# Kernel optimization log

Hardware: AMD Instinct MI355X
Metric: run time of the kernel (lower is better)

Reference implementation:

```python
import jax, jax.numpy as jnp
import numpy as np

D = 1024          # model_dim
BD = D // 2       # bottleneck_dim
K = 64            # num_splats
B, S = 8, 2048


def setup_inputs() -> dict:
    key = jax.random.key(0)
    ks = jax.random.split(key, 12)
    sc = 0.02
    return {
        "token_embeddings": jax.random.normal(ks[0], (B, S, D), jnp.float32),
        "splat_influences": jax.random.uniform(ks[1], (B, S, K), jnp.float32),
        # encoder: Linear(D -> BD), stored [in, out]
        "enc_W": jax.random.normal(ks[2], (D, BD), jnp.float32) * sc,
        "enc_b": jnp.zeros((BD,), jnp.float32),
        # per-splat transforms: K x Linear(BD -> BD)
        "trans_W": jax.random.normal(ks[3], (K, BD, BD), jnp.float32) * sc,
        "trans_b": jnp.zeros((K, BD), jnp.float32),
        # decoder: Linear(BD -> D)
        "dec_W": jax.random.normal(ks[4], (BD, D), jnp.float32) * sc,
        "dec_b": jnp.zeros((D,), jnp.float32),
        # flow gate: Linear(D -> D) + sigmoid
        "gate_W": jax.random.normal(ks[5], (D, D), jnp.float32) * sc,
        "gate_b": jnp.zeros((D,), jnp.float32),
    }


def reference(token_embeddings, splat_influences, enc_W, enc_b,
              trans_W, trans_b, dec_W, dec_b, gate_W, gate_b):
    # gather: [B,K,S] @ [B,S,D] -> [B,K,D]
    influences_t = jnp.swapaxes(splat_influences, 1, 2)          # [B,K,S]
    gathered = jnp.einsum('bks,bsd->bkd', influences_t, token_embeddings)
    total = jnp.clip(influences_t.sum(axis=2, keepdims=True), 1e-8, None)  # [B,K,1]
    gathered = gathered / total
    # encoder (dropout inactive at eval)
    encoded = jax.nn.relu(gathered @ enc_W + enc_b)              # [B,K,BD]
    # per-splat transform as grouped matmul
    transformed = jnp.einsum('bkd,kde->bke', encoded, trans_W) + trans_b  # [B,K,BD]
    decoded = transformed @ dec_W + dec_b                        # [B,K,D]
    # scatter back to tokens: [B,S,K] @ [B,K,D]
    flow = jnp.einsum('bsk,bkd->bsd', splat_influences, decoded)
    gate = jax.nn.sigmoid(token_embeddings @ gate_W + gate_b)    # [B,S,D]
    return flow * gate
```

## Files before the change

kernel.cpp:

```cpp
#include <hip/hip_runtime.h>

#define BB 8
#define SS 2048
#define DD 1024
#define BDD 512
#define NSP 64

typedef __attribute__((ext_vector_type(8))) short bf16x8;
typedef __attribute__((ext_vector_type(4))) float f32x4;
typedef unsigned short u16;
typedef unsigned int u32;

__device__ __forceinline__ u16 f2bf(float f) {
  u32 u = __builtin_bit_cast(u32, f);
  u = u + 0x7fffu + ((u >> 16) & 1u);
  return (u16)(u >> 16);
}

__device__ __forceinline__ void gl_lds16(const void* g, void* l) {
  __builtin_amdgcn_global_load_lds((const __attribute__((address_space(1))) void*)g,
                                   (__attribute__((address_space(3))) void*)l,
                                   16, 0, 0);
}

__global__ void k_prep(const float* __restrict__ tok, const float* __restrict__ infl,
                       const float* __restrict__ gw, u16* __restrict__ tokbf,
                       u16* __restrict__ tokT, u16* __restrict__ inflbf,
                       u16* __restrict__ inflT, float* __restrict__ rsum,
                       u16* __restrict__ gwt) {
  __shared__ __align__(16) char smraw[128 * 41 * 4];
  u16(*tile)[80] = (u16(*)[80])smraw;
  float(*ps)[64] = (float(*)[64])(smraw + 64 * 80 * 2);
  float(*gt)[33] = (float(*)[33])smraw;
  int bid = blockIdx.x;
  int t = threadIdx.x;

  if (bid < 2048) {
    u32* t32 = (u32*)smraw;
    int C0 = (bid & 15) * 64;
    int R0 = (bid >> 4) * 128;
    int b = R0 >> 11, s0 = R0 & 2047;
    int lc = (t & 7) * 8;
#pragma unroll
    for (int i = 0; i < 4; ++i) {
      int r = (t >> 3) + i * 32;
      const float* src = tok + (size_t)(R0 + r) * DD + C0 + lc;
      float4 a = *(const float4*)src;
      float4 bq = *(const float4*)(src + 4);
      uint4 v;
      v.x = f2bf(a.x) | ((u32)f2bf(a.y) << 16);
      v.y = f2bf(a.z) | ((u32)f2bf(a.w) << 16);
      v.z = f2bf(bq.x) | ((u32)f2bf(bq.y) << 16);
      v.w = f2bf(bq.z) | ((u32)f2bf(bq.w) << 16);
      *(uint4*)(tokbf + (size_t)(R0 + r) * DD + C0 + lc) = v;
      int cbase = r * 41 + (t & 7) * 4;
      t32[cbase + 0] = v.x;
      t32[cbase + 1] = v.y;
      t32[cbase + 2] = v.z;
      t32[cbase + 3] = v.w;
    }
    __syncthreads();
    int dp = t >> 3;
    size_t tb = (size_t)b * DD * SS;
#pragma unroll
    for (int h = 0; h < 2; ++h) {
      int sseg = (t & 7) * 8 + h * 64;
      u32 w[8];
#pragma unroll
      for (int j = 0; j < 8; ++j) w[j] = t32[(sseg + j) * 41 + dp];
      uint4 vlo, vhi;
      vlo.x = (w[0] & 0xffffu) | (w[1] << 16);
      vlo.y = (w[2] & 0xffffu) | (w[3] << 16);
      vlo.z = (w[4] & 0xffffu) | (w[5] << 16);
      vlo.w = (w[6] & 0xffffu) | (w[7] << 16);
      vhi.x = (w[0] >> 16) | (w[1] & 0xffff0000u);
      vhi.y = (w[2] >> 16) | (w[3] & 0xffff0000u);
      vhi.z = (w[4] >> 16) | (w[5] & 0xffff0000u);
      vhi.w = (w[6] >> 16) | (w[7] & 0xffff0000u);
      *(uint4*)(tokT + tb + (size_t)(C0 + 2 * dp) * SS + s0 + sseg) = vlo;
      *(uint4*)(tokT + tb + (size_t)(C0 + 2 * dp + 1) * SS + s0 + sseg) = vhi;
    }
  } else if (bid < 2304) {
    int R0 = (bid - 2048) * 64;
    int b = R0 >> 11, s0 = R0 & 2047;
    int st = s0 >> 6;
    int lr = t >> 3, lc = (t & 7) * 8;
    float col[8];
#pragma unroll
    for (int j = 0; j < 8; ++j) col[j] = 0.f;
#pragma unroll
    for (int i = 0; i < 2; ++i) {
      int r = lr + i * 32;
      const float* src = infl + (size_t)(R0 + r) * NSP + lc;
      float4 a = *(const float4*)src;
      float4 bq = *(const float4*)(src + 4);
      col[0] += a.x; col[1] += a.y; col[2] += a.z; col[3] += a.w;
      col[4] += bq.x; col[5] += bq.y; col[6] += bq.z; col[7] += bq.w;
      uint4 v;
      v.x = f2bf(a.x) | ((u32)f2bf(a.y) << 16);
      v.y = f2bf(a.z) | ((u32)f2bf(a.w) << 16);
      v.z = f2bf(bq.x) | ((u32)f2bf(bq.y) << 16);
      v.w = f2bf(bq.z) | ((u32)f2bf(bq.w) << 16);
      *(uint4*)(inflbf + (size_t)(R0 + r) * NSP + lc) = v;
      *(uint4*)&tile[r][lc] = v;
    }
#pragma unroll
    for (int j = 0; j < 8; ++j) ps[lr][lc + j] = col[j];
    __syncthreads();
    if (t < 64) {
      float s = 0.f;
#pragma unroll
      for (int rr = 0; rr < 32; ++rr) s += ps[rr][t];
      rsum[((size_t)b * 32 + st) * 64 + t] = s;
    }
    int sseg = (t & 7) * 8;
#pragma unroll
    for (int i = 0; i < 2; ++i) {
      int dcol = (t >> 3) + i * 32;
      u16 a0 = tile[sseg + 0][dcol], a1 = tile[sseg + 1][dcol];
      u16 a2 = tile[sseg + 2][dcol], a3 = tile[sseg + 3][dcol];
      u16 a4 = tile[sseg + 4][dcol], a5 = tile[sseg + 5][dcol];
      u16 a6 = tile[sseg + 6][dcol], a7 = tile[sseg + 7][dcol];
      uint4 v;
      v.x = a0 | ((u32)a1 << 16);
      v.y = a2 | ((u32)a3 << 16);
      v.z = a4 | ((u32)a5 << 16);
      v.w = a6 | ((u32)a7 << 16);
      *(uint4*)(inflT + ((size_t)b * NSP + dcol) * SS + s0 + sseg) = v;
    }
  } else {
    int g = bid - 2304;
    int n0 = (g & 31) * 32, k0 = (g >> 5) * 32;
    int tx = t & 31, ty = t >> 5;
#pragma unroll
    for (int r = 0; r < 4; ++r) {
      int kr = ty + r * 8;
      gt[kr][tx] = gw[(k0 + kr) * DD + n0 + tx];
    }
    __syncthreads();
#pragma unroll
    for (int r = 0; r < 4; ++r) {
      int nc = ty + r * 8;
      gwt[(n0 + nc) * DD + k0 + tx] = f2bf(gt[tx][nc]);
    }
  }
}

__global__ __launch_bounds__(256) void k_gather_mfma(const u16* __restrict__ inflT,
                                                     const u16* __restrict__ tokT,
                                                     float* __restrict__ pg) {
  __shared__ u16 As[64 * 64];
  __shared__ u16 Bs[64 * 64];
  int t = threadIdx.x;
  int l = t & 63, w = t >> 6;
  int wr = w >> 1, wc = w & 1;
  int n0 = blockIdx.x * 64;
  int b = blockIdx.y;
  int sq = blockIdx.z;
  int l15 = l & 15, lh = l >> 4;
  int srow = t >> 3, scol = (t & 7) * 8;

  const u16* ap = inflT + (size_t)b * NSP * SS;
  const u16* bp = tokT + (size_t)b * DD * SS;

  f32x4 acc[2][2];
#pragma unroll
  for (int i = 0; i < 2; ++i)
#pragma unroll
    for (int j = 0; j < 2; ++j) acc[i][j] = (f32x4){0.f, 0.f, 0.f, 0.f};

  for (int kt = 0; kt < 8; ++kt) {
    int k0 = sq * 512 + kt * 64;
#pragma unroll
    for (int i = 0; i < 2; ++i) {
      int row = srow + i * 32;
      gl_lds16(ap + row * SS + k0 + scol, &As[row * 64 + scol]);
      gl_lds16(bp + (n0 + row) * SS + k0 + scol, &Bs[row * 64 + scol]);
    }
    __syncthreads();
#pragma unroll
    for (int ks = 0; ks < 2; ++ks) {
      bf16x8 af[2], bfv[2];
#pragma unroll
      for (int mi = 0; mi < 2; ++mi)
        af[mi] = *(const bf16x8*)&As[(wr * 32 + mi * 16 + l15) * 64 + ks * 32 + lh * 8];
#pragma unroll
      for (int ni = 0; ni < 2; ++ni)
        bfv[ni] = *(const bf16x8*)&Bs[(wc * 32 + ni * 16 + l15) * 64 + ks * 32 + lh * 8];
#pragma unroll
      for (int mi = 0; mi < 2; ++mi)
#pragma unroll
        for (int ni = 0; ni < 2; ++ni)
          acc[mi][ni] = __builtin_amdgcn_mfma_f32_16x16x32_bf16(af[mi], bfv[ni], acc[mi][ni], 0, 0, 0);
    }
    __syncthreads();
  }

#pragma unroll
  for (int mi = 0; mi < 2; ++mi)
#pragma unroll
    for (int ni = 0; ni < 2; ++ni)
#pragma unroll
      for (int r = 0; r < 4; ++r) {
        int krow = wr * 32 + mi * 16 + lh * 4 + r;
        int dcol = n0 + wc * 32 + ni * 16 + l15;
        pg[((size_t)sq * 512 + b * NSP + krow) * DD + dcol] = acc[mi][ni][r];
      }
}

__global__ void k_enc_part(const float* __restrict__ pg, const float* __restrict__ rsum,
                           const float* __restrict__ encW, float* __restrict__ pe) {
  __shared__ float gl[8][64];
  int dq = blockIdx.x, mt = blockIdx.y;
  int m0 = mt * 8, d0 = dq * 64;
  int t = threadIdx.x;
  {
    int r = t >> 5, c = t & 31;
    float s1 = 0.f, s2 = 0.f;
#pragma unroll
    for (int q = 0; q < 4; ++q) {
      const float* qp = pg + ((size_t)q * 512 + m0 + r) * DD + d0;
      s1 += qp[c]; s2 += qp[c + 32];
    }
    int mrow = m0 + r;
    int bq = mrow >> 6, kq = mrow & 63;
    float tt = 0.f;
#pragma unroll
    for (int st = 0; st < 32; ++st) tt += rsum[((size_t)bq * 32 + st) * 64 + kq];
    float rt = 1.f / fmaxf(tt, 1e-8f);
    gl[r][c] = s1 * rt;
    gl[r][c + 32] = s2 * rt;
  }
  __syncthreads();
  int n4 = (t & 127) * 4, mh = (t >> 7) * 4;
  float4 acc[4];
#pragma unroll
  for (int m = 0; m < 4; ++m) acc[m] = (float4){0.f, 0.f, 0.f, 0.f};
  for (int i = 0; i < 64; ++i) {
    float4 wv = *(const float4*)(encW + (d0 + i) * BDD + n4);
#pragma unroll
    for (int m = 0; m < 4; ++m) {
      float g = gl[mh + m][i];
      acc[m].x += g * wv.x; acc[m].y += g * wv.y;
      acc[m].z += g * wv.z; acc[m].w += g * wv.w;
    }
  }
#pragma unroll
  for (int m = 0; m < 4; ++m)
    *(float4*)(pe + ((size_t)dq * 512 + m0 + mh + m) * BDD + n4) = acc[m];
}

__global__ void k_trans_part(const float* __restrict__ pe, const float* __restrict__ encB,
                             const float* __restrict__ trW, float* __restrict__ pt) {
  __shared__ float el[8][32];
  int dq = blockIdx.x, ks = blockIdx.y;
  int d0 = dq * 32;
  int t = threadIdx.x;
  {
    int r = t >> 5, c = t & 31;
    int m = r * NSP + ks;
    float s = 0.f;
#pragma unroll
    for (int p = 0; p < 16; ++p)
      s += pe[((size_t)p * 512 + m) * BDD + d0 + c];
    el[r][c] = fmaxf(s + encB[d0 + c], 0.f);
  }
  __syncthreads();
  int n4 = (t & 127) * 4, mh = (t >> 7) * 4;
  float4 acc[4];
#pragma unroll
  for (int m = 0; m < 4; ++m) acc[m] = (float4){0.f, 0.f, 0.f, 0.f};
  for (int i = 0; i < 32; ++i) {
    float4 wv = *(const float4*)(trW + ((size_t)ks * BDD + d0 + i) * BDD + n4);
#pragma unroll
    for (int m = 0; m < 4; ++m) {
      float g = el[mh + m][i];
      acc[m].x += g * wv.x; acc[m].y += g * wv.y;
      acc[m].z += g * wv.z; acc[m].w += g * wv.w;
    }
  }
#pragma unroll
  for (int m = 0; m < 4; ++m)
    *(float4*)(pt + ((size_t)dq * 512 + (mh + m) * NSP + ks) * BDD + n4) = acc[m];
}

__global__ void k_dec_part(const float* __restrict__ pt, const float* __restrict__ trB,
                           const float* __restrict__ decW, float* __restrict__ pd) {
  __shared__ float tl[8][64];
  int dq = blockIdx.x, mt = blockIdx.y;
  int m0 = mt * 8, d0 = dq * 64;
  int t = threadIdx.x;
  {
    int r = t >> 5, c = t & 31;
    int m = m0 + r;
    float s1 = 0.f, s2 = 0.f;
#pragma unroll
    for (int p = 0; p < 16; ++p) {
      const float* qp = pt + ((size_t)p * 512 + m) * BDD + d0;
      s1 += qp[c]; s2 += qp[c + 32];
    }
    tl[r][c] = s1 + trB[(m & 63) * BDD + d0 + c];
    tl[r][c + 32] = s2 + trB[(m & 63) * BDD + d0 + c + 32];
  }
  __syncthreads();
  int n4 = t * 4;
  float4 acc[8];
#pragma unroll
  for (int m = 0; m < 8; ++m) acc[m] = (float4){0.f, 0.f, 0.f, 0.f};
  for (int i = 0; i < 64; ++i) {
    float4 wv = *(const float4*)(decW + (d0 + i) * DD + n4);
#pragma unroll
    for (int m = 0; m < 8; ++m) {
      float g = tl[m][i];
      acc[m].x += g * wv.x; acc[m].y += g * wv.y;
      acc[m].z += g * wv.z; acc[m].w += g * wv.w;
    }
  }
#pragma unroll
  for (int m = 0; m < 8; ++m)
    *(float4*)(pd + ((size_t)dq * 512 + m0 + m) * DD + n4) = acc[m];
}

__global__ void red_dec(const float* __restrict__ pd, const float* __restrict__ decB,
                        u16* __restrict__ decT) {
  __shared__ u16 st[64][34];
  int nt = blockIdx.x, b = blockIdx.y;
  int n0 = nt * 32;
  int t = threadIdx.x;
  int nn = t & 31, kg = t >> 5;
  float db = decB[n0 + nn];
#pragma unroll
  for (int ki = 0; ki < 8; ++ki) {
    int ks = kg * 8 + ki;
    float s = db;
#pragma unroll
    for (int p = 0; p < 8; ++p)
      s += pd[((size_t)p * 512 + b * NSP + ks) * DD + n0 + nn];
    st[ks][nn] = f2bf(s);
  }
  __syncthreads();
  int nr = t >> 3, kseg = (t & 7) * 8;
  uint4 v;
  v.x = st[kseg + 0][nr] | ((u32)st[kseg + 1][nr] << 16);
  v.y = st[kseg + 2][nr] | ((u32)st[kseg + 3][nr] << 16);
  v.z = st[kseg + 4][nr] | ((u32)st[kseg + 5][nr] << 16);
  v.w = st[kseg + 6][nr] | ((u32)st[kseg + 7][nr] << 16);
  *(uint4*)(decT + ((size_t)b * DD + n0 + nr) * NSP + kseg) = v;
}


#define GVM(n) asm volatile("s_waitcnt vmcnt(" #n ")" ::: "memory");

#define GSTA(sl, k0, p)                                                        \
  { int e = (p)*512 + t; int row = e >> 3; int cs = ((e & 7) ^ (row & 7)) * 8; \
    gl_lds16(tokbf + (size_t)(m0 + row) * DD + (k0) + cs, &As[sl][e * 8]); }
#define GSTB(sl, k0, p)                                                        \
  { int e = (p)*512 + t; int row = e >> 3; int cs = ((e & 7) ^ (row & 7)) * 8; \
    gl_lds16(gwt + (size_t)(n0 + row) * DD + (k0) + cs, &Bs[sl][e * 8]); }

#define GLOADB(sl)                                                             \
  _Pragma("unroll")                                                            \
  for (int nf = 0; nf < 2; ++nf) {                                             \
    int br = wc * 32 + nf * 16 + l15;                                          \
    bfv[nf][0] = *(const bf16x8*)&Bs[sl][br * 64 + c0];                        \
    bfv[nf][1] = *(const bf16x8*)&Bs[sl][br * 64 + c1];                        \
  }

#define GPH(sl, mq, VMW, STG, LDB)                                             \
  {                                                                            \
    VMW                                                                        \
    __builtin_amdgcn_s_barrier();                                              \
    LDB                                                                        \
    bf16x8 af[4][2];                                                           \
    _Pragma("unroll")                                                          \
    for (int mf = 0; mf < 4; ++mf) {                                           \
      int ar = (mq)*64 + mf * 16 + l15;                                        \
      af[mf][0] = *(const bf16x8*)&As[sl][ar * 64 + c0];                       \
      af[mf][1] = *(const bf16x8*)&As[sl][ar * 64 + c1];                       \
    }                                                                          \
    STG                                                                        \
    __builtin_amdgcn_s_setprio(1);                                             \
    _Pragma("unroll")                                                          \
    for (int mf = 0; mf < 4; ++mf)                                             \
      _Pragma("unroll")                                                        \
      for (int nf = 0; nf < 2; ++nf) {                                         \
        acc[(mq)*4 + mf][nf] = __builtin_amdgcn_mfma_f32_16x16x32_bf16(af[mf][0], bfv[nf][0], acc[(mq)*4 + mf][nf], 0, 0, 0); \
        acc[(mq)*4 + mf][nf] = __builtin_amdgcn_mfma_f32_16x16x32_bf16(af[mf][1], bfv[nf][1], acc[(mq)*4 + mf][nf], 0, 0, 0); \
      }                                                                        \
    __builtin_amdgcn_s_setprio(0);                                             \
    __builtin_amdgcn_s_barrier();                                              \
  }

#define GT_FULL(sl, osl, k1)                                                   \
  {                                                                            \
    bf16x8 bfv[2][2];                                                          \
    GPH(sl, 0, GVM(3), GSTB(osl, k1, 0) GSTB(osl, k1, 1), GLOADB(sl))          \
    GPH(sl, 1, GVM(4), GSTB(osl, k1, 2) GSTB(osl, k1, 3), )                    \
    GPH(sl, 2, GVM(5), GSTA(osl, k1, 0) GSTA(osl, k1, 1), )                    \
    GPH(sl, 3, GVM(6), GSTA(osl, k1, 2) GSTA(osl, k1, 3), )                    \
  }
#define GT_LAST(sl)                                                            \
  {                                                                            \
    bf16x8 bfv[2][2];                                                          \
    GPH(sl, 0, GVM(3), , GLOADB(sl))                                           \
    GPH(sl, 1, GVM(2), , )                                                     \
    GPH(sl, 2, GVM(1), , )                                                     \
    GPH(sl, 3, GVM(0), , )                                                     \
  }

__global__ __launch_bounds__(512, 2) void k_gate(const u16* __restrict__ tokbf,
                                                 const u16* __restrict__ gwt,
                                                 u16* __restrict__ zbf) {
  __shared__ u16 As[2][256 * 64];
  __shared__ u16 Bs[2][256 * 64];
  int t = threadIdx.x;
  int l = t & 63, wc = t >> 6;
  int bid = blockIdx.x;
  int wg = (bid & 7) * 32 + (bid >> 3);
  int mt = wg & 63, nt = wg >> 6;
  int m0 = mt * 256, n0 = nt * 256;
  int l15 = l & 15, lh = l >> 4;
  int x7 = l15 & 7;
  int c0 = (lh ^ x7) * 8;
  int c1 = ((4 + lh) ^ x7) * 8;

  f32x4 acc[16][2];
#pragma unroll
  for (int i = 0; i < 16; ++i)
#pragma unroll
    for (int j = 0; j < 2; ++j) acc[i][j] = (f32x4){0.f, 0.f, 0.f, 0.f};

  GSTB(0, 0, 0) GSTB(0, 0, 1) GSTB(0, 0, 2) GSTB(0, 0, 3)
  GSTA(0, 0, 0) GSTA(0, 0, 1) GSTA(0, 0, 2) GSTA(0, 0, 3)

#pragma unroll 1
  for (int i = 0; i < 7; ++i) {
    GT_FULL(0, 1, (2 * i + 1) * 64)
    GT_FULL(1, 0, (2 * i + 2) * 64)
  }
  GT_FULL(0, 1, 960)
  GT_LAST(1)

#pragma unroll
  for (int a = 0; a < 16; ++a)
#pragma unroll
    for (int nf = 0; nf < 2; ++nf)
#pragma unroll
      for (int r = 0; r < 4; ++r) {
        int mr = m0 + a * 16 + lh * 4 + r;
        int nc = n0 + wc * 32 + nf * 16 + l15;
        zbf[(size_t)mr * DD + nc] = f2bf(acc[a][nf][r]);
      }
}

__global__ __launch_bounds__(256) void k_scat(const u16* __restrict__ inflbf,
                                              const u16* __restrict__ decT,
                                              const u16* __restrict__ zbf,
                                              const float* __restrict__ gateB,
                                              float* __restrict__ outp) {
  __shared__ u16 As[128 * 64];
  __shared__ u16 Bs[128 * 64];
  int t = threadIdx.x;
  int l = t & 63, w = t >> 6;
  int wr = w >> 1, wc = w & 1;
  int m0 = blockIdx.x * 128, n0 = blockIdx.y * 128;
  int l15 = l & 15, lh = l >> 4;
  int b = m0 >> 11, s0m = m0 & 2047;

#pragma unroll
  for (int i = 0; i < 4; ++i) {
    int row = i * 32 + (t >> 3);
    int cs = ((t & 7) ^ (row & 7)) * 8;
    gl_lds16(inflbf + ((size_t)b * SS + s0m + row) * NSP + cs, &As[i * 2048 + t * 8]);
  }
#pragma unroll
  for (int i = 0; i < 4; ++i) {
    int row = i * 32 + (t >> 3);
    int cs = ((t & 7) ^ (row & 7)) * 8;
    gl_lds16(decT + ((size_t)b * DD + n0 + row) * NSP + cs, &Bs[i * 2048 + t * 8]);
  }
  asm volatile("s_waitcnt vmcnt(0)" ::: "memory");
  __builtin_amdgcn_s_barrier();

  f32x4 accf[4][4];
#pragma unroll
  for (int i = 0; i < 4; ++i)
#pragma unroll
    for (int j = 0; j < 4; ++j) accf[i][j] = (f32x4){0.f, 0.f, 0.f, 0.f};
#pragma unroll
  for (int ks = 0; ks < 2; ++ks) {
    bf16x8 af[4], bfv[4];
    int g = ks * 4 + lh;
#pragma unroll
    for (int mi = 0; mi < 4; ++mi) {
      int r = wr * 64 + mi * 16 + l15;
      af[mi] = *(const bf16x8*)&As[r * 64 + (g ^ (r & 7)) * 8];
    }
#pragma unroll
    for (int ni = 0; ni < 4; ++ni) {
      int r = wc * 64 + ni * 16 + l15;
      bfv[ni] = *(const bf16x8*)&Bs[r * 64 + (g ^ (r & 7)) * 8];
    }
#pragma unroll
    for (int mi = 0; mi < 4; ++mi)
#pragma unroll
      for (int ni = 0; ni < 4; ++ni)
        accf[mi][ni] = __builtin_amdgcn_mfma_f32_16x16x32_bf16(af[mi], bfv[ni], accf[mi][ni], 0, 0, 0);
  }

  float gb[4];
#pragma unroll
  for (int ni = 0; ni < 4; ++ni) gb[ni] = gateB[n0 + wc * 64 + ni * 16 + l15];
#pragma unroll
  for (int mi = 0; mi < 4; ++mi)
#pragma unroll
    for (int ni = 0; ni < 4; ++ni)
#pragma unroll
      for (int r = 0; r < 4; ++r) {
        int mr = m0 + wr * 64 + mi * 16 + lh * 4 + r;
        int nc = n0 + wc * 64 + ni * 16 + l15;
        u16 zr = zbf[(size_t)mr * DD + nc];
        float z = __builtin_bit_cast(float, (u32)zr << 16) + gb[ni];
        float gate = 1.f / (1.f + __expf(-z));
        outp[(size_t)mr * DD + nc] = accf[mi][ni][r] * gate;
      }
}

extern "C" void kernel_launch(void* const* d_in, const int* in_sizes, int n_in,
                              void* d_out, int out_size, void* d_ws, size_t ws_size,
                              hipStream_t stream) {
  const float* tok = (const float*)d_in[0];
  const float* infl = (const float*)d_in[1];
  const float* encW = (const float*)d_in[2];
  const float* encB = (const float*)d_in[3];
  const float* trW = (const float*)d_in[4];
  const float* trB = (const float*)d_in[5];
  const float* decW = (const float*)d_in[6];
  const float* decB = (const float*)d_in[7];
  const float* gw = (const float*)d_in[8];
  const float* gateB = (const float*)d_in[9];
  float* outp = (float*)d_out;

  char* wsp = (char*)d_ws;
  u16* tokbf = (u16*)(wsp);
  u16* gwt = (u16*)(wsp + 33554432);
  u16* inflbf = (u16*)(wsp + 35651584);
  u16* decT = (u16*)(wsp + 41945088);
  u16* tokT = (u16*)(wsp + 42993664);
  float* pe = (float*)(wsp + 42993664);
  float* pt = (float*)(wsp + 42993664 + 16777216);
  u16* zbf = (u16*)(wsp + 42993664);
  u16* inflT = (u16*)(wsp + 76548096);
  float* rsum = (float*)(wsp + 78645248);
  float* scratch = (float*)(wsp + 78710784);

  k_prep<<<dim3(3328), dim3(256), 0, stream>>>(tok, infl, gw, tokbf, tokT, inflbf,
                                               inflT, rsum, gwt);
  k_gather_mfma<<<dim3(16, 8, 4), dim3(256), 0, stream>>>(inflT, tokT, scratch);
  k_enc_part<<<dim3(16, 64), dim3(256), 0, stream>>>(scratch, rsum, encW, pe);
  k_trans_part<<<dim3(16, 64), dim3(256), 0, stream>>>(pe, encB, trW, pt);
  k_dec_part<<<dim3(8, 64), dim3(256), 0, stream>>>(pt, trB, decW, scratch);
  red_dec<<<dim3(32, 8), dim3(256), 0, stream>>>(scratch, decB, decT);
  k_gate<<<dim3(256), dim3(512), 0, stream>>>(tokbf, gwt, zbf);
  k_scat<<<dim3(128, 8), dim3(256), 0, stream>>>(inflbf, decT, zbf, gateB, outp);
}
```

Before: 172.0 us.

## Fuse scatter GEMM and gating epilogue into gate GEMM kernel

The separate scatter kernel is removed. Each gate-GEMM block now keeps its gate pre-activations in registers as packed bf16, reloads its influence and decoded tiles into LDS, and runs the K=64 scatter matmul by reusing the GEMM phase macro. It then applies sigmoid and multiplies in the same epilogue. This avoids writing and re-reading the 32MB bf16 gate intermediate and saves one kernel launch. In exchange, the launch bound drops to one block per CU and register pressure rises from holding the packed z values alongside the accumulators.

After: 170.3 us. No clear change (-1.0%).

```diff
diff --git a/kernel.cpp b/kernel.cpp
--- a/kernel.cpp
+++ b/kernel.cpp
@@ -357,6 +357,12 @@
 #define GSTB(sl, k0, p)                                                        \
   { int e = (p)*512 + t; int row = e >> 3; int cs = ((e & 7) ^ (row & 7)) * 8; \
     gl_lds16(gwt + (size_t)(n0 + row) * DD + (k0) + cs, &Bs[sl][e * 8]); }
+#define SAI(sl, p)                                                             \
+  { int e = (p)*512 + t; int row = e >> 3; int cs = ((e & 7) ^ (row & 7)) * 8; \
+    gl_lds16(inflbf + ((size_t)bb * SS + s0m + row) * NSP + cs, &As[sl][e * 8]); }
+#define SBD(sl, p)                                                             \
+  { int e = (p)*512 + t; int row = e >> 3; int cs = ((e & 7) ^ (row & 7)) * 8; \
+    gl_lds16(decT + ((size_t)bb * DD + n0 + row) * NSP + cs, &Bs[sl][e * 8]); }
 
 #define GLOADB(sl)                                                             \
   _Pragma("unroll")                                                            \
@@ -407,10 +413,21 @@
     GPH(sl, 2, GVM(1), , )                                                     \
     GPH(sl, 3, GVM(0), , )                                                     \
   }
-
-__global__ __launch_bounds__(512, 2) void k_gate(const u16* __restrict__ tokbf,
+#define GT_SCAT(sl)                                                            \
+  {                                                                            \
+    bf16x8 bfv[2][2];                                                          \
+    GPH(sl, 0, , , GLOADB(sl))                                                 \
+    GPH(sl, 1, , , )                                                           \
+    GPH(sl, 2, , , )                                                           \
+    GPH(sl, 3, , , )                                                           \
+  }
+
+__global__ __launch_bounds__(512, 1) void k_gate(const u16* __restrict__ tokbf,
                                                  const u16* __restrict__ gwt,
-                                                 u16* __restrict__ zbf) {
+                                                 const u16* __restrict__ inflbf,
+                                                 const u16* __restrict__ decT,
+                                                 const float* __restrict__ gateB,
+                                                 float* __restrict__ outp) {
   __shared__ u16 As[2][256 * 64];
   __shared__ u16 Bs[2][256 * 64];
   int t = threadIdx.x;
@@ -423,6 +440,7 @@
   int x7 = l15 & 7;
   int c0 = (lh ^ x7) * 8;
   int c1 = ((4 + lh) ^ x7) * 8;
+  int bb = m0 >> 11, s0m = m0 & 2047;
 
   f32x4 acc[16][2];
 #pragma unroll
@@ -441,6 +459,29 @@
   GT_FULL(0, 1, 960)
   GT_LAST(1)
 
+  SAI(0, 0) SAI(0, 1) SAI(0, 2) SAI(0, 3)
+  SBD(0, 0) SBD(0, 1) SBD(0, 2) SBD(0, 3)
+
+  u32 zp[16][2][2];
+#pragma unroll
+  for (int a = 0; a < 16; ++a)
+#pragma unroll
+    for (int nf = 0; nf < 2; ++nf) {
+      zp[a][nf][0] = f2bf(acc[a][nf][0]) | ((u32)f2bf(acc[a][nf][1]) << 16);
+      zp[a][nf][1] = f2bf(acc[a][nf][2]) | ((u32)f2bf(acc[a][nf][3]) << 16);
+    }
+#pragma unroll
+  for (int i = 0; i < 16; ++i)
+#pragma unroll
+    for (int j = 0; j < 2; ++j) acc[i][j] = (f32x4){0.f, 0.f, 0.f, 0.f};
+  GVM(0)
+  __builtin_amdgcn_s_barrier();
+
+  GT_SCAT(0)
+
+  float gb[2];
+#pragma unroll
+  for (int nf = 0; nf < 2; ++nf) gb[nf] = gateB[n0 + wc * 32 + nf * 16 + l15];
 #pragma unroll
   for (int a = 0; a < 16; ++a)
 #pragma unroll
@@ -449,80 +490,11 @@
       for (int r = 0; r < 4; ++r) {
         int mr = m0 + a * 16 + lh * 4 + r;
         int nc = n0 + wc * 32 + nf * 16 + l15;
-        zbf[(size_t)mr * DD + nc] = f2bf(acc[a][nf][r]);
-      }
-}
-
-__global__ __launch_bounds__(256) void k_scat(const u16* __restrict__ inflbf,
-                                              const u16* __restrict__ decT,
-                                              const u16* __restrict__ zbf,
-                                              const float* __restrict__ gateB,
-                                              float* __restrict__ outp) {
-  __shared__ u16 As[128 * 64];
-  __shared__ u16 Bs[128 * 64];
-  int t = threadIdx.x;
-  int l = t & 63, w = t >> 6;
-  int wr = w >> 1, wc = w & 1;
-  int m0 = blockIdx.x * 128, n0 = blockIdx.y * 128;
-  int l15 = l & 15, lh = l >> 4;
-  int b = m0 >> 11, s0m = m0 & 2047;
-
-#pragma unroll
-  for (int i = 0; i < 4; ++i) {
-    int row = i * 32 + (t >> 3);
-    int cs = ((t & 7) ^ (row & 7)) * 8;
-    gl_lds16(inflbf + ((size_t)b * SS + s0m + row) * NSP + cs, &As[i * 2048 + t * 8]);
-  }
-#pragma unroll
-  for (int i = 0; i < 4; ++i) {
-    int row = i * 32 + (t >> 3);
-    int cs = ((t & 7) ^ (row & 7)) * 8;
-    gl_lds16(decT + ((size_t)b * DD + n0 + row) * NSP + cs, &Bs[i * 2048 + t * 8]);
-  }
-  asm volatile("s_waitcnt vmcnt(0)" ::: "memory");
-  __builtin_amdgcn_s_barrier();
-
-  f32x4 accf[4][4];
-#pragma unroll
-  for (int i = 0; i < 4; ++i)
-#pragma unroll
-    for (int j = 0; j < 4; ++j) accf[i][j] = (f32x4){0.f, 0.f, 0.f, 0.f};
-#pragma unroll
-  for (int ks = 0; ks < 2; ++ks) {
-    bf16x8 af[4], bfv[4];
-    int g = ks * 4 + lh;
-#pragma unroll
-    for (int mi = 0; mi < 4; ++mi) {
-      int r = wr * 64 + mi * 16 + l15;
-      af[mi] = *(const bf16x8*)&As[r * 64 + (g ^ (r & 7)) * 8];
-    }
-#pragma unroll
-    for (int ni = 0; ni < 4; ++ni) {
-      int r = wc * 64 + ni * 16 + l15;
-      bfv[ni] = *(const bf16x8*)&Bs[r * 64 + (g ^ (r & 7)) * 8];
-    }
-#pragma unroll
-    for (int mi = 0; mi < 4; ++mi)
-#pragma unroll
-      for (int ni = 0; ni < 4; ++ni)
-        accf[mi][ni] = __builtin_amdgcn_mfma_f32_16x16x32_bf16(af[mi], bfv[ni], accf[mi][ni], 0, 0, 0);
-  }
-
-  float gb[4];
-#pragma unroll
-  for (int ni = 0; ni < 4; ++ni) gb[ni] = gateB[n0 + wc * 64 + ni * 16 + l15];
-#pragma unroll
-  for (int mi = 0; mi < 4; ++mi)
-#pragma unroll
-    for (int ni = 0; ni < 4; ++ni)
-#pragma unroll
-      for (int r = 0; r < 4; ++r) {
-        int mr = m0 + wr * 64 + mi * 16 + lh * 4 + r;
-        int nc = n0 + wc * 64 + ni * 16 + l15;
-        u16 zr = zbf[(size_t)mr * DD + nc];
-        float z = __builtin_bit_cast(float, (u32)zr << 16) + gb[ni];
+        u32 wz = zp[a][nf][r >> 1];
+        u32 h = (r & 1) ? (wz & 0xffff0000u) : (wz << 16);
+        float z = __builtin_bit_cast(float, h) + gb[nf];
         float gate = 1.f / (1.f + __expf(-z));
-        outp[(size_t)mr * DD + nc] = accf[mi][ni][r] * gate;
+        outp[(size_t)mr * DD + nc] = acc[a][nf][r] * gate;
       }
 }
 
@@ -549,7 +521,6 @@
   u16* tokT = (u16*)(wsp + 42993664);
   float* pe = (float*)(wsp + 42993664);
   float* pt = (float*)(wsp + 42993664 + 16777216);
-  u16* zbf = (u16*)(wsp + 42993664);
   u16* inflT = (u16*)(wsp + 76548096);
   float* rsum = (float*)(wsp + 78645248);
   float* scratch = (float*)(wsp + 78710784);
@@ -561,6 +532,5 @@
   k_trans_part<<<dim3(16, 64), dim3(256), 0, stream>>>(pe, encB, trW, pt);
   k_dec_part<<<dim3(8, 64), dim3(256), 0, stream>>>(pt, trB, decW, scratch);
   red_dec<<<dim3(32, 8), dim3(256), 0, stream>>>(scratch, decB, decT);
-  k_gate<<<dim3(256), dim3(512), 0, stream>>>(tokbf, gwt, zbf);
-  k_scat<<<dim3(128, 8), dim3(256), 0, stream>>>(inflbf, decT, zbf, gateB, outp);
-}
+  k_gate<<<dim3(256), dim3(512), 0, stream>>>(tokbf, gwt, inflbf, decT, gateB, outp);
+}
```
